# Kernel tuning notes

Measured on AMD Instinct MI355X. Metric: run time of the kernel, lower is better.

Reference implementation:

```python
import jax, jax.numpy as jnp
import numpy as np

D_MODEL, D_STATE, D_CONV, EXPAND, DT_RANK = 1024, 16, 4, 2, 64
D_INNER = EXPAND * D_MODEL
B, L = 2, 4096


def setup_inputs() -> dict:
    key = jax.random.key(0)
    ks = jax.random.split(key, 9)
    s = 0.02
    x = jax.random.normal(ks[0], (B, L, D_MODEL), dtype=jnp.float32)
    in_proj_w = jax.random.normal(ks[1], (D_MODEL, 2 * D_INNER), dtype=jnp.float32) * s
    conv_w = jax.random.normal(ks[2], (D_INNER, 1, D_CONV), dtype=jnp.float32) * s
    conv_b = jnp.zeros((D_INNER,), dtype=jnp.float32)
    x_proj_w = jax.random.normal(ks[3], (D_INNER, DT_RANK + 2 * D_STATE), dtype=jnp.float32) * s
    dt_proj_w = jax.random.normal(ks[4], (DT_RANK, D_INNER), dtype=jnp.float32) * s
    # dt bias -> softplus(dt) roughly in [1e-3, 1e-1] as in mamba init
    dt = jnp.exp(jax.random.uniform(ks[5], (D_INNER,)) * (np.log(0.1) - np.log(1e-3)) + np.log(1e-3))
    dt_proj_b = (dt + jnp.log(-jnp.expm1(-dt))).astype(jnp.float32)  # inverse softplus
    A_log = jnp.log(jnp.broadcast_to(jnp.arange(1, D_STATE + 1, dtype=jnp.float32), (D_INNER, D_STATE)))
    Dp = jnp.ones((D_INNER,), dtype=jnp.float32)
    out_proj_w = jax.random.normal(ks[6], (D_INNER, D_MODEL), dtype=jnp.float32) * s
    return {"x": x, "in_proj_w": in_proj_w, "conv_w": conv_w, "conv_b": conv_b,
            "x_proj_w": x_proj_w, "dt_proj_w": dt_proj_w, "dt_proj_b": dt_proj_b,
            "A_log": A_log, "Dp": Dp, "out_proj_w": out_proj_w}


def _mamba(x, in_proj_w, conv_w, conv_b, x_proj_w, dt_proj_w, dt_proj_b, A_log, Dp, out_proj_w):
    # in projection -> (u, z), each [B, L, D_INNER]
    xz = jnp.einsum('bld,de->ble', x, in_proj_w)
    u, z = jnp.split(xz, 2, axis=-1)
    # causal depthwise conv1d over time
    u_c = jax.lax.conv_general_dilated(
        u.transpose(0, 2, 1), conv_w, window_strides=(1,),
        padding=[(D_CONV - 1, 0)],
        dimension_numbers=('NCH', 'OIH', 'NCH'),
        feature_group_count=D_INNER)
    u_c = jax.nn.silu(u_c.transpose(0, 2, 1) + conv_b)  # [B, L, D_INNER]
    # input-dependent dt, B, C
    dbc = jnp.einsum('bld,dr->blr', u_c, x_proj_w)
    dt_lo, Bc, Cc = jnp.split(dbc, [DT_RANK, DT_RANK + D_STATE], axis=-1)
    dt = jax.nn.softplus(jnp.einsum('blr,rd->bld', dt_lo, dt_proj_w) + dt_proj_b)  # [B,L,Di]
    A = -jnp.exp(A_log)  # [Di, N]

    def step(h, inp):
        u_t, dt_t, B_t, C_t = inp  # [B,Di],[B,Di],[B,N],[B,N]
        dA = jnp.exp(dt_t[..., None] * A)                      # [B,Di,N]
        h = h * dA + (dt_t * u_t)[..., None] * B_t[:, None, :]  # [B,Di,N]
        y = jnp.einsum('bdn,bn->bd', h, C_t)                   # [B,Di]
        return h, y

    h0 = jnp.zeros((x.shape[0], D_INNER, D_STATE), dtype=x.dtype)
    xs = (u_c.transpose(1, 0, 2), dt.transpose(1, 0, 2),
          Bc.transpose(1, 0, 2), Cc.transpose(1, 0, 2))
    _, ys = jax.lax.scan(step, h0, xs)      # [L, B, Di]
    y = ys.transpose(1, 0, 2) + u_c * Dp    # skip connection
    y = y * jax.nn.silu(z)                  # gate
    return jnp.einsum('bld,de->ble', y, out_proj_w)


def reference(x, in_proj_w, conv_w, conv_b, x_proj_w, dt_proj_w, dt_proj_b, A_log, Dp, out_proj_w):
    return _mamba(x, in_proj_w, conv_w, conv_b, x_proj_w, dt_proj_w, dt_proj_b, A_log, Dp, out_proj_w)
```

## Files before the change

### kernel.cpp

```cpp
#include <hip/hip_runtime.h>
#include <hip/hip_bf16.h>
#include <math.h>

#define BSZ 2
#define LSEQ 4096
#define DMODEL 1024
#define DINNER 2048
#define NSTATE 16
#define DTRANK 64
#define MROWS (BSZ * LSEQ)
#define NCHUNK 64
#define CHUNK (LSEQ / NCHUNK)
#define XKS 8
#define XKCH (DINNER / XKS)

#if __has_builtin(__builtin_amdgcn_exp2f)
#define EXP2F(x) __builtin_amdgcn_exp2f(x)
#else
#define EXP2F(x) exp2f(x)
#endif
#define LOG2E 1.44269504088896f

typedef __attribute__((ext_vector_type(8))) short bf16x8;
typedef __attribute__((ext_vector_type(4))) float f32x4;

__device__ __forceinline__ float sigmoidf_(float x) { return 1.0f / (1.0f + __expf(-x)); }

__device__ __forceinline__ unsigned short f2bf(float x) {
    unsigned int u = __float_as_uint(x);
    u += 0x7fff + ((u >> 16) & 1);
    return (unsigned short)(u >> 16);
}
__device__ __forceinline__ float bf2f(unsigned short b) {
    return __uint_as_float(((unsigned int)b) << 16);
}

__global__ __launch_bounds__(256) void cvt_swz_kernel(
    const float* __restrict__ X, unsigned short* __restrict__ Xb,
    int logGpr)
{
    int gid = blockIdx.x * 256 + threadIdx.x;
    int m = gid >> logGpr;
    int g = gid & ((1 << logGpr) - 1);
    int K = 8 << logGpr;
    size_t src = (size_t)m * K + g * 8;
    float4 v0 = *reinterpret_cast<const float4*>(X + src);
    float4 v1 = *reinterpret_cast<const float4*>(X + src + 4);
    unsigned int w0 = (unsigned)f2bf(v0.x) | ((unsigned)f2bf(v0.y) << 16);
    unsigned int w1 = (unsigned)f2bf(v0.z) | ((unsigned)f2bf(v0.w) << 16);
    unsigned int w2 = (unsigned)f2bf(v1.x) | ((unsigned)f2bf(v1.y) << 16);
    unsigned int w3 = (unsigned)f2bf(v1.z) | ((unsigned)f2bf(v1.w) << 16);
    size_t dst = (size_t)m * K + ((g * 8) ^ ((m & 7) << 3));
    uint4 w = {w0, w1, w2, w3};
    *reinterpret_cast<uint4*>(Xb + dst) = w;
}

__global__ __launch_bounds__(256) void transpose_swz_kernel(
    const float* __restrict__ W, unsigned short* __restrict__ WT, int K, int Nsrc)
{
    __shared__ float tile[64][65];
    const int t = threadIdx.x;
    const int n0 = blockIdx.x * 64;
    const int k0 = blockIdx.y * 64;

    #pragma unroll
    for (int i = 0; i < 16; ++i) {
        int flat = i * 256 + t;
        int r = flat >> 6, c = flat & 63;
        tile[r][c] = (n0 + c < Nsrc) ? W[(size_t)(k0 + r) * Nsrc + n0 + c] : 0.0f;
    }
    __syncthreads();
    #pragma unroll
    for (int i = 0; i < 16; ++i) {
        int flat = i * 256 + t;
        int n = flat >> 6, k = flat & 63;
        int ks = k ^ ((n & 7) << 3);
        WT[(size_t)(n0 + n) * K + k0 + ks] = f2bf(tile[k][n]);
    }
}

template<int OBF>
__global__ __launch_bounds__(256) void gemm_bb_kernel(
    const unsigned short* __restrict__ Abf, const unsigned short* __restrict__ BT,
    void* __restrict__ Cv, int M, int N, int K, int ldc)
{
    __shared__ unsigned short lds_a[128 * 64];
    __shared__ unsigned short lds_b[128 * 64];

    const int tid  = threadIdx.x;
    const int lane = tid & 63;
    const int w    = tid >> 6;
    const int wr   = (w >> 1) * 64;
    const int wc   = (w & 1) * 64;
    const int row0 = blockIdx.y * 128;
    const int col0 = blockIdx.x * 128;

    f32x4 acc[4][4];
    #pragma unroll
    for (int m = 0; m < 4; ++m)
        #pragma unroll
        for (int n = 0; n < 4; ++n)
            acc[m][n] = (f32x4){0.f, 0.f, 0.f, 0.f};

    for (int k0 = 0; k0 < K; k0 += 64) {
        #pragma unroll
        for (int j = 0; j < 4; ++j) {
            int c  = (j * 4 + w) * 64 + lane;
            int r  = c >> 3;
            int cc = c & 7;
            const char* asrc = (const char*)Abf +
                ((size_t)(row0 + r) * K + k0) * 2 + cc * 16;
            __builtin_amdgcn_global_load_lds(
                (const __attribute__((address_space(1))) void*)asrc,
                (__attribute__((address_space(3))) void*)((char*)lds_a + (j * 4 + w) * 1024),
                16, 0, 0);
            const char* bsrc = (const char*)BT +
                ((size_t)(col0 + r) * K + k0) * 2 + cc * 16;
            __builtin_amdgcn_global_load_lds(
                (const __attribute__((address_space(1))) void*)bsrc,
                (__attribute__((address_space(3))) void*)((char*)lds_b + (j * 4 + w) * 1024),
                16, 0, 0);
        }
        __syncthreads();

        #pragma unroll
        for (int kk = 0; kk < 2; ++kk) {
            bf16x8 af[4], bfr[4];
            #pragma unroll
            for (int m = 0; m < 4; ++m) {
                int r = wr + m * 16 + (lane & 15);
                int byteoff = r * 128 + ((kk * 64 + (lane >> 4) * 16) ^ ((r & 7) << 4));
                af[m] = *reinterpret_cast<const bf16x8*>((const char*)lds_a + byteoff);
            }
            #pragma unroll
            for (int n = 0; n < 4; ++n) {
                int r = wc + n * 16 + (lane & 15);
                int byteoff = r * 128 + ((kk * 64 + (lane >> 4) * 16) ^ ((r & 7) << 4));
                bfr[n] = *reinterpret_cast<const bf16x8*>((const char*)lds_b + byteoff);
            }
            #pragma unroll
            for (int m = 0; m < 4; ++m)
                #pragma unroll
                for (int n = 0; n < 4; ++n)
                    acc[m][n] = __builtin_amdgcn_mfma_f32_16x16x32_bf16(
                        af[m], bfr[n], acc[m][n], 0, 0, 0);
        }
        __syncthreads();
    }

    #pragma unroll
    for (int m = 0; m < 4; ++m) {
        int rbase = row0 + wr + m * 16 + (lane >> 4) * 4;
        #pragma unroll
        for (int n = 0; n < 4; ++n) {
            int col = col0 + wc + n * 16 + (lane & 15);
            #pragma unroll
            for (int r = 0; r < 4; ++r) {
                if (OBF) {
                    ((unsigned short*)Cv)[(size_t)(rbase + r) * ldc + col] =
                        f2bf(acc[m][n][r]);
                } else {
                    ((float*)Cv)[(size_t)(rbase + r) * ldc + col] = acc[m][n][r];
                }
            }
        }
    }
}

__global__ __launch_bounds__(256) void xproj_splitk_bb_kernel(
    const unsigned short* __restrict__ Abf, const unsigned short* __restrict__ BT,
    float* __restrict__ part)
{
    __shared__ unsigned short lds_a[128 * 64];
    __shared__ unsigned short lds_b[128 * 64];

    const int tid  = threadIdx.x;
    const int lane = tid & 63;
    const int w    = tid >> 6;
    const int wr   = (w >> 1) * 64;
    const int wc   = (w & 1) * 64;
    const int row0 = blockIdx.y * 128;
    const int kb   = blockIdx.z * XKCH;
    const int K    = DINNER;

    f32x4 acc[4][4];
    #pragma unroll
    for (int m = 0; m < 4; ++m)
        #pragma unroll
        for (int n = 0; n < 4; ++n)
            acc[m][n] = (f32x4){0.f, 0.f, 0.f, 0.f};

    for (int k0 = kb; k0 < kb + XKCH; k0 += 64) {
        #pragma unroll
        for (int j = 0; j < 4; ++j) {
            int c  = (j * 4 + w) * 64 + lane;
            int r  = c >> 3;
            int cc = c & 7;
            const char* asrc = (const char*)Abf +
                ((size_t)(row0 + r) * K + k0) * 2 + cc * 16;
            __builtin_amdgcn_global_load_lds(
                (const __attribute__((address_space(1))) void*)asrc,
                (__attribute__((address_space(3))) void*)((char*)lds_a + (j * 4 + w) * 1024),
                16, 0, 0);
            const char* bsrc = (const char*)BT +
                ((size_t)r * K + k0) * 2 + cc * 16;
            __builtin_amdgcn_global_load_lds(
                (const __attribute__((address_space(1))) void*)bsrc,
                (__attribute__((address_space(3))) void*)((char*)lds_b + (j * 4 + w) * 1024),
                16, 0, 0);
        }
        __syncthreads();

        #pragma unroll
        for (int kk = 0; kk < 2; ++kk) {
            bf16x8 af[4], bfr[4];
            #pragma unroll
            for (int m = 0; m < 4; ++m) {
                int r = wr + m * 16 + (lane & 15);
                int byteoff = r * 128 + ((kk * 64 + (lane >> 4) * 16) ^ ((r & 7) << 4));
                af[m] = *reinterpret_cast<const bf16x8*>((const char*)lds_a + byteoff);
            }
            #pragma unroll
            for (int n = 0; n < 4; ++n) {
                int r = wc + n * 16 + (lane & 15);
                int byteoff = r * 128 + ((kk * 64 + (lane >> 4) * 16) ^ ((r & 7) << 4));
                bfr[n] = *reinterpret_cast<const bf16x8*>((const char*)lds_b + byteoff);
            }
            #pragma unroll
            for (int m = 0; m < 4; ++m)
                #pragma unroll
                for (int n = 0; n < 4; ++n)
                    acc[m][n] = __builtin_amdgcn_mfma_f32_16x16x32_bf16(
                        af[m], bfr[n], acc[m][n], 0, 0, 0);
        }
        __syncthreads();
    }

    float* pbase = part + (size_t)blockIdx.z * MROWS * 96;
    #pragma unroll
    for (int m = 0; m < 4; ++m) {
        int rbase = row0 + wr + m * 16 + (lane >> 4) * 4;
        #pragma unroll
        for (int n = 0; n < 4; ++n) {
            int col = wc + n * 16 + (lane & 15);
            if (col < 96) {
                #pragma unroll
                for (int r = 0; r < 4; ++r)
                    pbase[(size_t)(rbase + r) * 96 + col] = acc[m][n][r];
            }
        }
    }
}

__global__ __launch_bounds__(256) void xproj_reduce_kernel(
    const float* __restrict__ part, float* __restrict__ dbc,
    unsigned short* __restrict__ dtlo)
{
    int gid = blockIdx.x * 256 + threadIdx.x;
    float s = 0.f;
    #pragma unroll
    for (int k = 0; k < XKS; ++k)
        s += part[(size_t)k * MROWS * 96 + gid];
    dbc[gid] = s;
    int row = gid / 96;
    int col = gid - row * 96;
    if (col < 64)
        dtlo[(size_t)row * 64 + (col ^ ((row & 7) << 3))] = f2bf(s);
}

__global__ __launch_bounds__(256) void gemm_dtproj_bb_kernel(
    const unsigned short* __restrict__ Abf, const unsigned short* __restrict__ BT,
    const float* __restrict__ bias, float* __restrict__ C)
{
    __shared__ unsigned short lds_a[128 * 64];
    __shared__ unsigned short lds_b[128 * 64];

    const int tid  = threadIdx.x;
    const int lane = tid & 63;
    const int w    = tid >> 6;
    const int wr   = (w >> 1) * 64;
    const int wc   = (w & 1) * 64;
    const int row0 = blockIdx.y * 128;
    const int col0 = blockIdx.x * 128;

    f32x4 acc[4][4];
    #pragma unroll
    for (int m = 0; m < 4; ++m)
        #pragma unroll
        for (int n = 0; n < 4; ++n)
            acc[m][n] = (f32x4){0.f, 0.f, 0.f, 0.f};

    #pragma unroll
    for (int j = 0; j < 4; ++j) {
        int c  = (j * 4 + w) * 64 + lane;
        int r  = c >> 3;
        int cc = c & 7;
        const char* asrc = (const char*)Abf + ((size_t)(row0 + r) * 64) * 2 + cc * 16;
        __builtin_amdgcn_global_load_lds(
            (const __attribute__((address_space(1))) void*)asrc,
            (__attribute__((address_space(3))) void*)((char*)lds_a + (j * 4 + w) * 1024),
            16, 0, 0);
        const char* bsrc = (const char*)BT + ((size_t)(col0 + r) * 64) * 2 + cc * 16;
        __builtin_amdgcn_global_load_lds(
            (const __attribute__((address_space(1))) void*)bsrc,
            (__attribute__((address_space(3))) void*)((char*)lds_b + (j * 4 + w) * 1024),
            16, 0, 0);
    }
    __syncthreads();

    #pragma unroll
    for (int kk = 0; kk < 2; ++kk) {
        bf16x8 af[4], bfr[4];
        #pragma unroll
        for (int m = 0; m < 4; ++m) {
            int r = wr + m * 16 + (lane & 15);
            int byteoff = r * 128 + ((kk * 64 + (lane >> 4) * 16) ^ ((r & 7) << 4));
            af[m] = *reinterpret_cast<const bf16x8*>((const char*)lds_a + byteoff);
        }
        #pragma unroll
        for (int n = 0; n < 4; ++n) {
            int r = wc + n * 16 + (lane & 15);
            int byteoff = r * 128 + ((kk * 64 + (lane >> 4) * 16) ^ ((r & 7) << 4));
            bfr[n] = *reinterpret_cast<const bf16x8*>((const char*)lds_b + byteoff);
        }
        #pragma unroll
        for (int m = 0; m < 4; ++m)
            #pragma unroll
            for (int n = 0; n < 4; ++n)
                acc[m][n] = __builtin_amdgcn_mfma_f32_16x16x32_bf16(
                    af[m], bfr[n], acc[m][n], 0, 0, 0);
    }

    #pragma unroll
    for (int m = 0; m < 4; ++m) {
        int rbase = row0 + wr + m * 16 + (lane >> 4) * 4;
        #pragma unroll
        for (int n = 0; n < 4; ++n) {
            int col = col0 + wc + n * 16 + (lane & 15);
            float bv = bias[col];
            #pragma unroll
            for (int r = 0; r < 4; ++r) {
                float v = acc[m][n][r] + bv;
                v = (v > 20.0f) ? v : log1pf(__expf(v));
                C[(size_t)(rbase + r) * DINNER + col] = v;
            }
        }
    }
}

__global__ __launch_bounds__(256) void conv_silu_kernel(
    const unsigned short* __restrict__ xzb, const float* __restrict__ cw,
    const float* __restrict__ cb, unsigned short* __restrict__ ucbf)
{
    int gid = blockIdx.x * 256 + threadIdx.x;
    int row = gid >> 8;
    int d0  = (gid & 255) * 8;
    int t = row & (LSEQ - 1);

    uint4 uv[4];
    #pragma unroll
    for (int k = 0; k < 4; ++k) {
        if (t - 3 + k >= 0)
            uv[k] = *reinterpret_cast<const uint4*>(
                xzb + (size_t)(row + k - 3) * 4096 + d0);
        else
            uv[k] = (uint4){0u, 0u, 0u, 0u};
    }

    float v[8];
    #pragma unroll
    for (int i = 0; i < 8; ++i) {
        float acc = cb[d0 + i];
        float4 wv = *reinterpret_cast<const float4*>(cw + (size_t)(d0 + i) * 4);
        float wk[4] = {wv.x, wv.y, wv.z, wv.w};
        #pragma unroll
        for (int k = 0; k < 4; ++k) {
            unsigned int word = (&uv[k].x)[i >> 1];
            float u = __uint_as_float((i & 1) ? (word & 0xffff0000u) : (word << 16));
            acc = fmaf(u, wk[k], acc);
        }
        v[i] = acc * sigmoidf_(acc);
    }

    uint4 o;
    o.x = (unsigned)f2bf(v[0]) | ((unsigned)f2bf(v[1]) << 16);
    o.y = (unsigned)f2bf(v[2]) | ((unsigned)f2bf(v[3]) << 16);
    o.z = (unsigned)f2bf(v[4]) | ((unsigned)f2bf(v[5]) << 16);
    o.w = (unsigned)f2bf(v[6]) | ((unsigned)f2bf(v[7]) << 16);
    *reinterpret_cast<uint4*>(
        ucbf + (size_t)row * DINNER + (d0 ^ ((row & 7) << 3))) = o;
}

__global__ __launch_bounds__(256) void scan_partial_kernel(
    const float* __restrict__ dtf, const unsigned short* __restrict__ ucbf,
    const float* __restrict__ dbc, const float* __restrict__ A_log,
    float* __restrict__ Pbuf, float* __restrict__ Ebuf)
{
    __shared__ float sB[CHUNK][NSTATE];
    const int tid = threadIdx.x;
    const int c = blockIdx.x;
    const int b = blockIdx.z;
    const int d = blockIdx.y * 256 + tid;
    const size_t row0 = (size_t)b * LSEQ + c * CHUNK;

    {
        int s = tid >> 2, f = tid & 3;
        float4 v = *reinterpret_cast<const float4*>(dbc + (row0 + s) * 96 + 64 + f * 4);
        *reinterpret_cast<float4*>(&sB[s][f * 4]) = v;
    }

    float An2[NSTATE];
    #pragma unroll
    for (int k = 0; k < 4; ++k) {
        float4 a = *reinterpret_cast<const float4*>(A_log + (size_t)d * NSTATE + k * 4);
        An2[k*4+0] = -__expf(a.x) * LOG2E;
        An2[k*4+1] = -__expf(a.y) * LOG2E;
        An2[k*4+2] = -__expf(a.z) * LOG2E;
        An2[k*4+3] = -__expf(a.w) * LOG2E;
    }
    __syncthreads();

    float E[NSTATE];
    #pragma unroll
    for (int n = 0; n < NSTATE; ++n) E[n] = 0.f;
    float S = 0.f;

    float dtc = dtf[row0 * DINNER + d];
    float ucv = bf2f(ucbf[row0 * DINNER + d]);
    for (int s = 0; s < CHUNK; ++s) {
        float dtn = 0.f, un = 0.f;
        if (s + 1 < CHUNK) {
            dtn = dtf[(row0 + s + 1) * DINNER + d];
            un  = bf2f(ucbf[(row0 + s + 1) * DINNER + (d ^ (((s + 1) & 7) << 3))]);
        }
        S += dtc;
        float du = dtc * ucv;
        float Bv[NSTATE];
        #pragma unroll
        for (int k = 0; k < 4; ++k)
            *reinterpret_cast<float4*>(&Bv[k*4]) =
                *reinterpret_cast<const float4*>(&sB[s][k*4]);
        #pragma unroll
        for (int n = 0; n < NSTATE; ++n) {
            float q = EXP2F(dtc * An2[n]);
            E[n] = fmaf(E[n], q, du * Bv[n]);
        }
        dtc = dtn; ucv = un;
    }

    size_t base = (((size_t)c * BSZ + b) * DINNER + d) * NSTATE;
    #pragma unroll
    for (int n = 0; n < NSTATE; ++n) {
        Pbuf[base + n] = EXP2F(An2[n] * S);
        Ebuf[base + n] = E[n];
    }
}

__global__ __launch_bounds__(256) void scan_prefix_kernel(
    float* __restrict__ Pbuf, const float* __restrict__ Ebuf)
{
    const int gid = blockIdx.x * 256 + threadIdx.x;
    const size_t stride = (size_t)BSZ * DINNER * NSTATE;
    size_t idx = gid;
    float h = 0.f;
    for (int c = 0; c < NCHUNK; ++c) {
        float P = Pbuf[idx];
        float Ev = Ebuf[idx];
        Pbuf[idx] = h;
        h = fmaf(P, h, Ev);
        idx += stride;
    }
}

__global__ __launch_bounds__(256) void scan_final_kernel(
    const float* __restrict__ dtf, const unsigned short* __restrict__ ucbf,
    const unsigned short* __restrict__ xzb, const float* __restrict__ dbc,
    const float* __restrict__ A_log, const float* __restrict__ Dp,
    const float* __restrict__ H0, unsigned short* __restrict__ ybf)
{
    __shared__ float sBC[CHUNK][2 * NSTATE];
    const int tid = threadIdx.x;
    const int c = blockIdx.x;
    const int b = blockIdx.z;
    const int d = blockIdx.y * 256 + tid;
    const size_t row0 = (size_t)b * LSEQ + c * CHUNK;

    {
        #pragma unroll
        for (int i = 0; i < 2; ++i) {
            int j = tid * 2 + i;
            int s = j >> 3, f = j & 7;
            float4 v = *reinterpret_cast<const float4*>(dbc + (row0 + s) * 96 + 64 + f * 4);
            *reinterpret_cast<float4*>(&sBC[s][f * 4]) = v;
        }
    }

    float An2[NSTATE];
    #pragma unroll
    for (int k = 0; k < 4; ++k) {
        float4 a = *reinterpret_cast<const float4*>(A_log + (size_t)d * NSTATE + k * 4);
        An2[k*4+0] = -__expf(a.x) * LOG2E;
        An2[k*4+1] = -__expf(a.y) * LOG2E;
        An2[k*4+2] = -__expf(a.z) * LOG2E;
        An2[k*4+3] = -__expf(a.w) * LOG2E;
    }
    const float Dpd = Dp[d];

    float h[NSTATE];
    {
        size_t base = (((size_t)c * BSZ + b) * DINNER + d) * NSTATE;
        #pragma unroll
        for (int n = 0; n < NSTATE; ++n) h[n] = H0[base + n];
    }
    __syncthreads();

    float dtc = dtf[row0 * DINNER + d];
    float ucv = bf2f(ucbf[row0 * DINNER + d]);
    float zc  = bf2f(xzb[row0 * 4096 + 2048 + d]);
    for (int s = 0; s < CHUNK; ++s) {
        float dtn = 0.f, un = 0.f, zn = 0.f;
        if (s + 1 < CHUNK) {
            dtn = dtf[(row0 + s + 1) * DINNER + d];
            un  = bf2f(ucbf[(row0 + s + 1) * DINNER + (d ^ (((s + 1) & 7) << 3))]);
            zn  = bf2f(xzb[(row0 + s + 1) * 4096 + 2048 + d]);
        }
        float du = dtc * ucv;
        float Bv[NSTATE], Cv[NSTATE];
        #pragma unroll
        for (int k = 0; k < 4; ++k) {
            *reinterpret_cast<float4*>(&Bv[k*4]) =
                *reinterpret_cast<const float4*>(&sBC[s][k*4]);
            *reinterpret_cast<float4*>(&Cv[k*4]) =
                *reinterpret_cast<const float4*>(&sBC[s][16 + k*4]);
        }
        float y0 = 0.f, y1 = 0.f, y2 = 0.f, y3 = 0.f;
        #pragma unroll
        for (int n = 0; n < NSTATE; ++n) {
            float q = EXP2F(dtc * An2[n]);
            h[n] = fmaf(h[n], q, du * Bv[n]);
            float& yk = (n & 3) == 0 ? y0 : (n & 3) == 1 ? y1 : (n & 3) == 2 ? y2 : y3;
            yk = fmaf(h[n], Cv[n], yk);
        }
        float y = (y0 + y1) + (y2 + y3);
        float yg = (y + ucv * Dpd) * (zc * sigmoidf_(zc));
        ybf[(row0 + s) * DINNER + (d ^ ((s & 7) << 3))] = f2bf(yg);
        dtc = dtn; ucv = un; zc = zn;
    }
}

extern "C" void kernel_launch(void* const* d_in, const int* in_sizes, int n_in,
                              void* d_out, int out_size, void* d_ws, size_t ws_size,
                              hipStream_t stream)
{
    const float* x         = (const float*)d_in[0];
    const float* in_proj_w = (const float*)d_in[1];
    const float* conv_w    = (const float*)d_in[2];
    const float* conv_b    = (const float*)d_in[3];
    const float* x_proj_w  = (const float*)d_in[4];
    const float* dt_proj_w = (const float*)d_in[5];
    const float* dt_proj_b = (const float*)d_in[6];
    const float* A_log     = (const float*)d_in[7];
    const float* Dp        = (const float*)d_in[8];
    const float* out_proj_w= (const float*)d_in[9];
    float* out = (float*)d_out;

    char* base = (char*)d_ws;
    unsigned short* xzb  = (unsigned short*)base;
    float* dtf           = (float*)(base + (64ull << 20));
    unsigned short* ucbf = (unsigned short*)(base + (128ull << 20));
    float* dbc           = (float*)(base + (160ull << 20));
    unsigned short* wT_in  = (unsigned short*)(base + (163ull << 20));
    unsigned short* wT_out = (unsigned short*)(base + (171ull << 20));
    unsigned short* wXT    = (unsigned short*)(base + (175ull << 20));
    unsigned short* wDT    = (unsigned short*)(base + (175ull << 20) + (512ull << 10));
    char* U = base + (176ull << 20);
    unsigned short* xbf  = (unsigned short*)U;
    float* part          = (float*)U;
    unsigned short* dtlo = (unsigned short*)(U + (24ull << 20));
    float* Pbuf          = (float*)(U + (16ull << 20));
    float* Ebuf          = (float*)(U + (32ull << 20));
    unsigned short* ybf  = (unsigned short*)(U + (32ull << 20));

    dim3 blk(256);

    cvt_swz_kernel<<<dim3(4096), blk, 0, stream>>>(x, xbf, 7);
    transpose_swz_kernel<<<dim3(64, 16), blk, 0, stream>>>(in_proj_w, wT_in, 1024, 4096);
    transpose_swz_kernel<<<dim3(16, 32), blk, 0, stream>>>(out_proj_w, wT_out, 2048, 1024);
    transpose_swz_kernel<<<dim3(2, 32),  blk, 0, stream>>>(x_proj_w,  wXT, 2048, 96);
    transpose_swz_kernel<<<dim3(32, 1),  blk, 0, stream>>>(dt_proj_w, wDT, 64, 2048);

    gemm_bb_kernel<1><<<dim3(32, 64), blk, 0, stream>>>(
        xbf, wT_in, (void*)xzb, MROWS, 4096, 1024, 4096);

    conv_silu_kernel<<<dim3((MROWS * (DINNER / 8)) / 256), blk, 0, stream>>>(
        xzb, conv_w, conv_b, ucbf);

    xproj_splitk_bb_kernel<<<dim3(1, 64, XKS), blk, 0, stream>>>(ucbf, wXT, part);
    xproj_reduce_kernel<<<dim3((MROWS * 96) / 256), blk, 0, stream>>>(part, dbc, dtlo);

    gemm_dtproj_bb_kernel<<<dim3(16, 64), blk, 0, stream>>>(dtlo, wDT, dt_proj_b, dtf);

    scan_partial_kernel<<<dim3(NCHUNK, DINNER / 256, BSZ), blk, 0, stream>>>(
        dtf, ucbf, dbc, A_log, Pbuf, Ebuf);
    scan_prefix_kernel<<<dim3((BSZ * DINNER * NSTATE) / 256), blk, 0, stream>>>(Pbuf, Ebuf);
    scan_final_kernel<<<dim3(NCHUNK, DINNER / 256, BSZ), blk, 0, stream>>>(
        dtf, ucbf, xzb, dbc, A_log, Dp, Pbuf, ybf);

    gemm_bb_kernel<0><<<dim3(8, 64), blk, 0, stream>>>(
        ybf, wT_out, (void*)out, MROWS, 1024, 2048, 1024);
}
```

Before: 435.2 us.

## Fuse prep kernels, swizzle GEMM workgroups across XCDs, store dt in bf16

Merges the input conversion and four weight transposes into one launch, dispatching on block id. Remaps GEMM workgroup ids so consecutive tiles land on the same XCD for better L2 reuse. Stores softplus(dt) as bf16 instead of fp32, halving dt traffic in the dt-proj writer and both scan kernels, and compacts the workspace layout. The bf16 dt loses precision in the exponent of the state decay, which could affect accuracy.

```diff
diff --git a/kernel.cpp b/kernel.cpp
--- a/kernel.cpp
+++ b/kernel.cpp
@@ -35,33 +35,42 @@
     return __uint_as_float(((unsigned int)b) << 16);
 }
 
-__global__ __launch_bounds__(256) void cvt_swz_kernel(
-    const float* __restrict__ X, unsigned short* __restrict__ Xb,
-    int logGpr)
-{
-    int gid = blockIdx.x * 256 + threadIdx.x;
-    int m = gid >> logGpr;
-    int g = gid & ((1 << logGpr) - 1);
-    int K = 8 << logGpr;
-    size_t src = (size_t)m * K + g * 8;
-    float4 v0 = *reinterpret_cast<const float4*>(X + src);
-    float4 v1 = *reinterpret_cast<const float4*>(X + src + 4);
-    unsigned int w0 = (unsigned)f2bf(v0.x) | ((unsigned)f2bf(v0.y) << 16);
-    unsigned int w1 = (unsigned)f2bf(v0.z) | ((unsigned)f2bf(v0.w) << 16);
-    unsigned int w2 = (unsigned)f2bf(v1.x) | ((unsigned)f2bf(v1.y) << 16);
-    unsigned int w3 = (unsigned)f2bf(v1.z) | ((unsigned)f2bf(v1.w) << 16);
-    size_t dst = (size_t)m * K + ((g * 8) ^ ((m & 7) << 3));
-    uint4 w = {w0, w1, w2, w3};
-    *reinterpret_cast<uint4*>(Xb + dst) = w;
-}
-
-__global__ __launch_bounds__(256) void transpose_swz_kernel(
-    const float* __restrict__ W, unsigned short* __restrict__ WT, int K, int Nsrc)
+__global__ __launch_bounds__(256) void prep_kernel(
+    const float* __restrict__ x, unsigned short* __restrict__ xbf,
+    const float* __restrict__ w_in, unsigned short* __restrict__ wT_in,
+    const float* __restrict__ w_out, unsigned short* __restrict__ wT_out,
+    const float* __restrict__ w_x, unsigned short* __restrict__ wXT,
+    const float* __restrict__ w_dt, unsigned short* __restrict__ wDT)
 {
     __shared__ float tile[64][65];
+    const int id = blockIdx.x;
     const int t = threadIdx.x;
-    const int n0 = blockIdx.x * 64;
-    const int k0 = blockIdx.y * 64;
+
+    if (id >= 1632) {
+        int gid = (id - 1632) * 256 + t;
+        int m = gid >> 7;
+        int g = gid & 127;
+        size_t src = (size_t)m * 1024 + g * 8;
+        float4 v0 = *reinterpret_cast<const float4*>(x + src);
+        float4 v1 = *reinterpret_cast<const float4*>(x + src + 4);
+        uint4 w;
+        w.x = (unsigned)f2bf(v0.x) | ((unsigned)f2bf(v0.y) << 16);
+        w.y = (unsigned)f2bf(v0.z) | ((unsigned)f2bf(v0.w) << 16);
+        w.z = (unsigned)f2bf(v1.x) | ((unsigned)f2bf(v1.y) << 16);
+        w.w = (unsigned)f2bf(v1.z) | ((unsigned)f2bf(v1.w) << 16);
+        size_t dst = (size_t)m * 1024 + ((g * 8) ^ ((m & 7) << 3));
+        *reinterpret_cast<uint4*>(xbf + dst) = w;
+        return;
+    }
+
+    const float* W; unsigned short* WT; int K, Nsrc, nb, kb;
+    if (id < 1024)      { W = w_in;  WT = wT_in;  K = 1024; Nsrc = 4096; nb = id & 63; kb = id >> 6; }
+    else if (id < 1536) { int q = id - 1024; W = w_out; WT = wT_out; K = 2048; Nsrc = 1024; nb = q & 15; kb = q >> 4; }
+    else if (id < 1600) { int q = id - 1536; W = w_x;   WT = wXT;   K = 2048; Nsrc = 96;   nb = q & 1;  kb = q >> 1; }
+    else                { int q = id - 1600; W = w_dt;  WT = wDT;   K = 64;   Nsrc = 2048; nb = q;      kb = 0; }
+
+    const int n0 = nb * 64;
+    const int k0 = kb * 64;
 
     #pragma unroll
     for (int i = 0; i < 16; ++i) {
@@ -87,13 +96,20 @@
     __shared__ unsigned short lds_a[128 * 64];
     __shared__ unsigned short lds_b[128 * 64];
 
+    const int nwg = gridDim.x * gridDim.y;
+    const int wg  = blockIdx.y * gridDim.x + blockIdx.x;
+    const int cpx = nwg >> 3;
+    const int swz = (wg & 7) * cpx + (wg >> 3);
+    const int bx  = swz % gridDim.x;
+    const int by  = swz / gridDim.x;
+
     const int tid  = threadIdx.x;
     const int lane = tid & 63;
     const int w    = tid >> 6;
     const int wr   = (w >> 1) * 64;
     const int wc   = (w & 1) * 64;
-    const int row0 = blockIdx.y * 128;
-    const int col0 = blockIdx.x * 128;
+    const int row0 = by * 128;
+    const int col0 = bx * 128;
 
     f32x4 acc[4][4];
     #pragma unroll
@@ -270,7 +286,7 @@
 
 __global__ __launch_bounds__(256) void gemm_dtproj_bb_kernel(
     const unsigned short* __restrict__ Abf, const unsigned short* __restrict__ BT,
-    const float* __restrict__ bias, float* __restrict__ C)
+    const float* __restrict__ bias, unsigned short* __restrict__ C)
 {
     __shared__ unsigned short lds_a[128 * 64];
     __shared__ unsigned short lds_b[128 * 64];
@@ -342,7 +358,7 @@
             for (int r = 0; r < 4; ++r) {
                 float v = acc[m][n][r] + bv;
                 v = (v > 20.0f) ? v : log1pf(__expf(v));
-                C[(size_t)(rbase + r) * DINNER + col] = v;
+                C[(size_t)(rbase + r) * DINNER + col] = f2bf(v);
             }
         }
     }
@@ -392,7 +408,7 @@
 }
 
 __global__ __launch_bounds__(256) void scan_partial_kernel(
-    const float* __restrict__ dtf, const unsigned short* __restrict__ ucbf,
+    const unsigned short* __restrict__ dtb, const unsigned short* __restrict__ ucbf,
     const float* __restrict__ dbc, const float* __restrict__ A_log,
     float* __restrict__ Pbuf, float* __restrict__ Ebuf)
 {
@@ -425,12 +441,12 @@
     for (int n = 0; n < NSTATE; ++n) E[n] = 0.f;
     float S = 0.f;
 
-    float dtc = dtf[row0 * DINNER + d];
+    float dtc = bf2f(dtb[row0 * DINNER + d]);
     float ucv = bf2f(ucbf[row0 * DINNER + d]);
     for (int s = 0; s < CHUNK; ++s) {
         float dtn = 0.f, un = 0.f;
         if (s + 1 < CHUNK) {
-            dtn = dtf[(row0 + s + 1) * DINNER + d];
+            dtn = bf2f(dtb[(row0 + s + 1) * DINNER + d]);
             un  = bf2f(ucbf[(row0 + s + 1) * DINNER + (d ^ (((s + 1) & 7) << 3))]);
         }
         S += dtc;
@@ -473,7 +489,7 @@
 }
 
 __global__ __launch_bounds__(256) void scan_final_kernel(
-    const float* __restrict__ dtf, const unsigned short* __restrict__ ucbf,
+    const unsigned short* __restrict__ dtb, const unsigned short* __restrict__ ucbf,
     const unsigned short* __restrict__ xzb, const float* __restrict__ dbc,
     const float* __restrict__ A_log, const float* __restrict__ Dp,
     const float* __restrict__ H0, unsigned short* __restrict__ ybf)
@@ -514,13 +530,13 @@
     }
     __syncthreads();
 
-    float dtc = dtf[row0 * DINNER + d];
+    float dtc = bf2f(dtb[row0 * DINNER + d]);
     float ucv = bf2f(ucbf[row0 * DINNER + d]);
     float zc  = bf2f(xzb[row0 * 4096 + 2048 + d]);
     for (int s = 0; s < CHUNK; ++s) {
         float dtn = 0.f, un = 0.f, zn = 0.f;
         if (s + 1 < CHUNK) {
-            dtn = dtf[(row0 + s + 1) * DINNER + d];
+            dtn = bf2f(dtb[(row0 + s + 1) * DINNER + d]);
             un  = bf2f(ucbf[(row0 + s + 1) * DINNER + (d ^ (((s + 1) & 7) << 3))]);
             zn  = bf2f(xzb[(row0 + s + 1) * 4096 + 2048 + d]);
         }
@@ -566,28 +582,25 @@
 
     char* base = (char*)d_ws;
     unsigned short* xzb  = (unsigned short*)base;
-    float* dtf           = (float*)(base + (64ull << 20));
-    unsigned short* ucbf = (unsigned short*)(base + (128ull << 20));
-    float* dbc           = (float*)(base + (160ull << 20));
-    unsigned short* wT_in  = (unsigned short*)(base + (163ull << 20));
-    unsigned short* wT_out = (unsigned short*)(base + (171ull << 20));
-    unsigned short* wXT    = (unsigned short*)(base + (175ull << 20));
-    unsigned short* wDT    = (unsigned short*)(base + (175ull << 20) + (512ull << 10));
-    char* U = base + (176ull << 20);
+    unsigned short* dtb  = (unsigned short*)(base + (64ull << 20));
+    unsigned short* ucbf = (unsigned short*)(base + (96ull << 20));
+    float* dbc           = (float*)(base + (128ull << 20));
+    unsigned short* wT_in  = (unsigned short*)(base + (131ull << 20));
+    unsigned short* wT_out = (unsigned short*)(base + (139ull << 20));
+    unsigned short* wXT    = (unsigned short*)(base + (143ull << 20));
+    unsigned short* wDT    = (unsigned short*)(base + (143ull << 20) + (512ull << 10));
+    char* U = base + (144ull << 20);
     unsigned short* xbf  = (unsigned short*)U;
     float* part          = (float*)U;
     unsigned short* dtlo = (unsigned short*)(U + (24ull << 20));
-    float* Pbuf          = (float*)(U + (16ull << 20));
-    float* Ebuf          = (float*)(U + (32ull << 20));
+    float* Pbuf          = (float*)U;
+    float* Ebuf          = (float*)(U + (16ull << 20));
     unsigned short* ybf  = (unsigned short*)(U + (32ull << 20));
 
     dim3 blk(256);
 
-    cvt_swz_kernel<<<dim3(4096), blk, 0, stream>>>(x, xbf, 7);
-    transpose_swz_kernel<<<dim3(64, 16), blk, 0, stream>>>(in_proj_w, wT_in, 1024, 4096);
-    transpose_swz_kernel<<<dim3(16, 32), blk, 0, stream>>>(out_proj_w, wT_out, 2048, 1024);
-    transpose_swz_kernel<<<dim3(2, 32),  blk, 0, stream>>>(x_proj_w,  wXT, 2048, 96);
-    transpose_swz_kernel<<<dim3(32, 1),  blk, 0, stream>>>(dt_proj_w, wDT, 64, 2048);
+    prep_kernel<<<dim3(5728), blk, 0, stream>>>(
+        x, xbf, in_proj_w, wT_in, out_proj_w, wT_out, x_proj_w, wXT, dt_proj_w, wDT);
 
     gemm_bb_kernel<1><<<dim3(32, 64), blk, 0, stream>>>(
         xbf, wT_in, (void*)xzb, MROWS, 4096, 1024, 4096);
@@ -598,13 +611,13 @@
     xproj_splitk_bb_kernel<<<dim3(1, 64, XKS), blk, 0, stream>>>(ucbf, wXT, part);
     xproj_reduce_kernel<<<dim3((MROWS * 96) / 256), blk, 0, stream>>>(part, dbc, dtlo);
 
-    gemm_dtproj_bb_kernel<<<dim3(16, 64), blk, 0, stream>>>(dtlo, wDT, dt_proj_b, dtf);
+    gemm_dtproj_bb_kernel<<<dim3(16, 64), blk, 0, stream>>>(dtlo, wDT, dt_proj_b, dtb);
 
     scan_partial_kernel<<<dim3(NCHUNK, DINNER / 256, BSZ), blk, 0, stream>>>(
-        dtf, ucbf, dbc, A_log, Pbuf, Ebuf);
+        dtb, ucbf, dbc, A_log, Pbuf, Ebuf);
     scan_prefix_kernel<<<dim3((BSZ * DINNER * NSTATE) / 256), blk, 0, stream>>>(Pbuf, Ebuf);
     scan_final_kernel<<<dim3(NCHUNK, DINNER / 256, BSZ), blk, 0, stream>>>(
-        dtf, ucbf, xzb, dbc, A_log, Dp, Pbuf, ybf);
+        dtb, ucbf, xzb, dbc, A_log, Dp, Pbuf, ybf);
 
     gemm_bb_kernel<0><<<dim3(8, 64), blk, 0, stream>>>(
         ybf, wT_out, (void*)out, MROWS, 1024, 2048, 1024);
```

After: 403.9 us. 1.08x faster.
